# Optimization experiments

Measured on AMD Instinct MI355X. Metric: run time of the kernel, lower is better.

## Reference

```python
import jax, jax.numpy as jnp
import numpy as np

IGNORE = jnp.float32(-100000.0)

N_HEADS, D_MODEL, D_HEAD = 12, 768, 64


def setup_inputs() -> dict:
    key = jax.random.key(0)
    ks = jax.random.split(key, 5)
    B, S = 2, 2048
    std = 0.02
    x = jax.random.normal(ks[0], (B, S, D_MODEL), dtype=jnp.float32)
    W_Q = jax.random.normal(ks[1], (N_HEADS, D_MODEL, D_HEAD), dtype=jnp.float32) * std
    W_K = jax.random.normal(ks[2], (N_HEADS, D_MODEL, D_HEAD), dtype=jnp.float32) * std
    W_V = jax.random.normal(ks[3], (N_HEADS, D_MODEL, D_HEAD), dtype=jnp.float32) * std
    W_O = jax.random.normal(ks[4], (N_HEADS, D_HEAD, D_MODEL), dtype=jnp.float32) * std
    b_Q = jnp.zeros((N_HEADS, D_HEAD), dtype=jnp.float32)
    b_K = jnp.zeros((N_HEADS, D_HEAD), dtype=jnp.float32)
    b_V = jnp.zeros((N_HEADS, D_HEAD), dtype=jnp.float32)
    b_O = jnp.zeros((D_MODEL,), dtype=jnp.float32)
    return {"normalized_resid_pre": x, "W_Q": W_Q, "W_K": W_K, "W_V": W_V,
            "b_Q": b_Q, "b_K": b_K, "b_V": b_V, "W_O": W_O, "b_O": b_O}


def reference(normalized_resid_pre, W_Q, W_K, W_V, b_Q, b_K, b_V, W_O, b_O):
    x = normalized_resid_pre  # [b, s, d_model]
    q = jnp.einsum('bsd,hdk->bshk', x, W_Q) + b_Q  # [b, s, h, d_head]
    k = jnp.einsum('bsd,hdk->bshk', x, W_K) + b_K
    v = jnp.einsum('bsd,hdk->bshk', x, W_V) + b_V
    scores = jnp.einsum('bqhk,bkhd->bhqk'.replace('d', 'x').replace('x', 'k'),
                        q, k) if False else jnp.einsum('bihd,bjhd->bhij', q, k)
    scores = scores / jnp.sqrt(jnp.float32(q.shape[-1]))
    S = scores.shape[-1]
    causal = jnp.tril(jnp.ones((S, S), dtype=bool))  # True = keep
    scores = jnp.where(causal, scores, IGNORE)
    attn = jax.nn.softmax(scores, axis=-1)  # [b, h, q, k]
    z = jnp.einsum('bhij,bjhd->bihd', attn, v)  # [b, s, h, d_head]
    out = jnp.einsum('bihd,hdm->bim', z, W_O) + b_O  # [b, s, d_model]
    return out
```

## Files before the change

kernel.cpp:

```cpp
#include <hip/hip_runtime.h>


#define DEVINL __device__ __forceinline__

using bf16x8 = __attribute__((ext_vector_type(8))) __bf16;
using f32x4  = __attribute__((ext_vector_type(4))) float;

DEVINL unsigned short f32_bf16(float f) {
    unsigned u = __builtin_bit_cast(unsigned, f);
    return (unsigned short)((u + 0x7FFFu + ((u >> 16) & 1u)) >> 16);
}

DEVINL void gload16(const void* g, void* l) {
    __builtin_amdgcn_global_load_lds(
        (const __attribute__((address_space(1))) void*)g,
        (__attribute__((address_space(3))) void*)l, 16, 0, 0);
}

__global__ __launch_bounds__(256) void k_prep(const float* __restrict__ x,
                                              const float* __restrict__ Wq,
                                              const float* __restrict__ Wk,
                                              const float* __restrict__ Wv,
                                              const float* __restrict__ Wo,
                                              unsigned short* __restrict__ xb,
                                              unsigned short* __restrict__ wqkvT,
                                              unsigned short* __restrict__ woT) {
    __shared__ unsigned short tl[64][68];
    const int bid = blockIdx.x;
    const int t = threadIdx.x;
    if (bid < 3072) {
        int i = (bid * 256 + t) * 4;
        float4 v = *(const float4*)(x + i);
        ushort4 o;
        o.x = f32_bf16(v.x); o.y = f32_bf16(v.y); o.z = f32_bf16(v.z); o.w = f32_bf16(v.w);
        *(ushort4*)(xb + i) = o;
        return;
    }
    const int c = t & 63, r0 = t >> 6;
    if (bid < 3504) {
        const int sub = bid - 3072;
        const int tr = sub % 12, batch = sub / 12;
        const float* src = (batch < 12) ? Wq : (batch < 24) ? Wk : Wv;
        src += (size_t)(batch % 12) * 768 * 64;
        unsigned short* out = wqkvT + (size_t)batch * 64 * 768;
#pragma unroll
        for (int k = 0; k < 16; ++k) {
            int r = k * 4 + r0;
            tl[r][c] = f32_bf16(src[(size_t)(tr * 64 + r) * 64 + c]);
        }
        __syncthreads();
#pragma unroll
        for (int k = 0; k < 16; ++k) {
            int r2 = k * 4 + r0;
            out[(size_t)r2 * 768 + tr * 64 + c] = tl[c][r2];
        }
    } else {
        const int sub = bid - 3504;
        const int tr = sub % 12, tc = sub / 12;
#pragma unroll
        for (int k = 0; k < 16; ++k) {
            int r = k * 4 + r0;
            tl[r][c] = f32_bf16(Wo[(size_t)(tr * 64 + r) * 768 + tc * 64 + c]);
        }
        __syncthreads();
#pragma unroll
        for (int k = 0; k < 16; ++k) {
            int r2 = k * 4 + r0;
            woT[(size_t)(tc * 64 + r2) * 768 + tr * 64 + c] = tl[c][r2];
        }
    }
}

template <int BM, int BN, bool QKV>
__global__ __launch_bounds__(256) void k_gemm(const unsigned short* __restrict__ A,
                                              const unsigned short* __restrict__ BT,
                                              const float* __restrict__ b0,
                                              const float* __restrict__ b1,
                                              const float* __restrict__ b2,
                                              unsigned short* __restrict__ outb,
                                              unsigned short* __restrict__ vtb,
                                              float* __restrict__ outf) {
    constexpr int LDC = QKV ? 2304 : 768;
    constexpr int WM = BM / 2, WN = BN / 2, MR = WM / 16, NR = WN / 16;
    __shared__ alignas(16) unsigned short As[2][BM * 64];
    __shared__ alignas(16) unsigned short Bs[2][BN * 64];
    const int t = threadIdx.x;
    const int w = t >> 6, l = t & 63, lr = l & 15, lg = l >> 4;
    const int wr = (w >> 1) * WM, wc = (w & 1) * WN;
    const int m0 = blockIdx.y * BM;
    const int n0 = blockIdx.x * BN;

    auto stage = [&](int buf, int kt) {
        const int k0 = kt * 64;
#pragma unroll
        for (int i = 0; i < BM / 32; ++i) {
            const int s = i * 256 + t;
            const int row = s >> 3, cs = (s & 7) ^ (row & 7);
            gload16((const char*)A + ((size_t)(m0 + row) * 768 + k0) * 2 + cs * 16,
                    (char*)As[buf] + s * 16);
        }
#pragma unroll
        for (int i = 0; i < BN / 32; ++i) {
            const int s = i * 256 + t;
            const int row = s >> 3, cs = (s & 7) ^ (row & 7);
            gload16((const char*)BT + ((size_t)(n0 + row) * 768 + k0) * 2 + cs * 16,
                    (char*)Bs[buf] + s * 16);
        }
    };

    stage(0, 0);
    __syncthreads();

    f32x4 acc[MR][NR] = {};

    for (int kt = 0; kt < 12; ++kt) {
        const int cur = kt & 1;
        if (kt < 11) stage(cur ^ 1, kt + 1);

        bf16x8 af[MR][2], bfr[NR][2];
#pragma unroll
        for (int ri = 0; ri < MR; ++ri)
#pragma unroll
            for (int kk = 0; kk < 2; ++kk)
                af[ri][kk] = *(const bf16x8*)&As[cur][(wr + ri * 16 + lr) * 64 +
                                                     (((kk * 4 + lg) ^ (lr & 7)) << 3)];
#pragma unroll
        for (int cj = 0; cj < NR; ++cj)
#pragma unroll
            for (int kk = 0; kk < 2; ++kk)
                bfr[cj][kk] = *(const bf16x8*)&Bs[cur][(wc + cj * 16 + lr) * 64 +
                                                       (((kk * 4 + lg) ^ (lr & 7)) << 3)];
        __builtin_amdgcn_s_setprio(1);
#pragma unroll
        for (int ri = 0; ri < MR; ++ri)
#pragma unroll
            for (int cj = 0; cj < NR; ++cj) {
                acc[ri][cj] = __builtin_amdgcn_mfma_f32_16x16x32_bf16(
                    af[ri][0], bfr[cj][0], acc[ri][cj], 0, 0, 0);
                acc[ri][cj] = __builtin_amdgcn_mfma_f32_16x16x32_bf16(
                    af[ri][1], bfr[cj][1], acc[ri][cj], 0, 0, 0);
            }
        __builtin_amdgcn_s_setprio(0);
        __syncthreads();
    }

#pragma unroll
    for (int cj = 0; cj < NR; ++cj) {
        const int col = n0 + wc + cj * 16 + lr;
        if (QKV && col >= 1536) {
            const int vc = col - 1536;
            const float bv = b2[vc];
            const int hh = vc >> 6, dd = vc & 63;
#pragma unroll
            for (int ri = 0; ri < MR; ++ri) {
                const int row = m0 + wr + ri * 16 + lg * 4;
                const int bb = row >> 11, s = row & 2047;
                ushort4 pkv;
                pkv.x = f32_bf16(acc[ri][cj][0] + bv);
                pkv.y = f32_bf16(acc[ri][cj][1] + bv);
                pkv.z = f32_bf16(acc[ri][cj][2] + bv);
                pkv.w = f32_bf16(acc[ri][cj][3] + bv);
                *(ushort4*)(vtb + ((size_t)(bb * 12 + hh) * 64 + dd) * 2048 + s) = pkv;
            }
        } else {
            const float* bp = b0;
            int cc = col;
            if (QKV && col >= 768) { bp = b1; cc = col - 768; }
            const float bv = bp[cc];
            const float scl = (QKV && col < 768) ? 0.18033688011112042f : 1.0f;
#pragma unroll
            for (int ri = 0; ri < MR; ++ri)
#pragma unroll
                for (int e = 0; e < 4; ++e) {
                    const int row = m0 + wr + ri * 16 + lg * 4 + e;
                    const float v = (acc[ri][cj][e] + bv) * scl;
                    if (QKV) outb[(size_t)row * LDC + col] = f32_bf16(v);
                    else     outf[(size_t)row * LDC + col] = v;
                }
        }
    }
}

#define WREG 8704
__global__ __launch_bounds__(256) void k_flash(const unsigned short* __restrict__ qkv,
                                               const unsigned short* __restrict__ vtb,
                                               unsigned short* __restrict__ zb) {
    __shared__ alignas(16) char smem[4 * WREG + 1024];
    const int hb = blockIdx.x;
    const int h = hb % 12, b = hb / 12;
    const int p = blockIdx.y;
    const int qiA = 32 + p, qiB = 31 - p;
    const int q0A = qiA * 32, q0B = qiB * 32;
    const int nkvA = (qiA >> 1) + 1, nkvB = (qiB >> 1) + 1;
    const int t = threadIdx.x, w = t >> 6, l = t & 63, lr = l & 15, lg = l >> 4;

    char* p_w = smem + w * WREG;
    float* lldsA = (float*)(smem + 4 * WREG);
    float* lldsB = (float*)(smem + 4 * WREG + 512);

    const size_t qrowbase = (size_t)(b * 2048) * 2304;
    bf16x8 qfA[2][2], qfB[2][2];
#pragma unroll
    for (int ri = 0; ri < 2; ++ri)
#pragma unroll
        for (int kk = 0; kk < 2; ++kk) {
            qfA[ri][kk] = *(const bf16x8*)(qkv + qrowbase +
                                           (size_t)(q0A + ri * 16 + lr) * 2304 +
                                           h * 64 + kk * 32 + lg * 8);
            qfB[ri][kk] = *(const bf16x8*)(qkv + qrowbase +
                                           (size_t)(q0B + ri * 16 + lr) * 2304 +
                                           h * 64 + kk * 32 + lg * 8);
        }

    f32x4 oA[2][4] = {}, oB[2][4] = {};
    float lsA[2] = {0.f, 0.f}, lsB[2] = {0.f, 0.f};

    const unsigned short* kb = qkv + qrowbase + 768 + h * 64;
    const unsigned short* vt = vtb + (size_t)(b * 12 + h) * 64 * 2048;

    {
        bf16x8 kf[4][2];
        auto loadK = [&](int kv0) {
#pragma unroll
            for (int cj = 0; cj < 4; ++cj)
#pragma unroll
                for (int kk = 0; kk < 2; ++kk)
                    kf[cj][kk] = *(const bf16x8*)(kb + (size_t)(kv0 + cj * 16 + lr) * 2304 +
                                                  kk * 32 + lg * 8);
        };

        int kt = w;
        loadK(kt * 64);
        do {
            const int kv0 = kt * 64;

            bf16x8 vf[2][4];
#pragma unroll
            for (int kk = 0; kk < 2; ++kk)
#pragma unroll
                for (int dj = 0; dj < 4; ++dj)
                    vf[kk][dj] = *(const bf16x8*)(vt + (size_t)(dj * 16 + lr) * 2048 +
                                                  kv0 + kk * 32 + lg * 8);

            const f32x4 zz = {0.f, 0.f, 0.f, 0.f};

            if (kt < nkvB) {
                f32x4 st[2][4];
                __builtin_amdgcn_s_setprio(1);
#pragma unroll
                for (int ri = 0; ri < 2; ++ri)
#pragma unroll
                    for (int cj = 0; cj < 4; ++cj) {
                        f32x4 a0 = __builtin_amdgcn_mfma_f32_16x16x32_bf16(kf[cj][0], qfB[ri][0], zz, 0, 0, 0);
                        st[ri][cj] = __builtin_amdgcn_mfma_f32_16x16x32_bf16(kf[cj][1], qfB[ri][1], a0, 0, 0, 0);
                    }
                __builtin_amdgcn_s_setprio(0);

                if (kt == nkvB - 1) {
#pragma unroll
                    for (int ri = 0; ri < 2; ++ri)
#pragma unroll
                        for (int cj = 0; cj < 4; ++cj)
#pragma unroll
                            for (int e = 0; e < 4; ++e) {
                                const int kvv = kv0 + cj * 16 + lg * 4 + e;
                                const int qq  = q0B + ri * 16 + lr;
                                if (kvv > qq) st[ri][cj][e] = -1e30f;
                            }
                }

#pragma unroll
                for (int ri = 0; ri < 2; ++ri) {
                    float ps = 0.f;
#pragma unroll
                    for (int cj = 0; cj < 4; ++cj)
#pragma unroll
                        for (int e = 0; e < 4; ++e) {
                            const float pv = __builtin_amdgcn_exp2f(st[ri][cj][e]);
                            st[ri][cj][e] = pv;
                            ps += pv;
                        }
                    lsB[ri] += ps;

                    const int row = ri * 16 + lr;
#pragma unroll
                    for (int cj = 0; cj < 4; ++cj) {
                        unsigned lo, hi;
                        asm("v_cvt_pk_bf16_f32 %0, %1, %2"
                            : "=v"(lo) : "v"(st[ri][cj][0]), "v"(st[ri][cj][1]));
                        asm("v_cvt_pk_bf16_f32 %0, %1, %2"
                            : "=v"(hi) : "v"(st[ri][cj][2]), "v"(st[ri][cj][3]));
                        const int gr = (cj * 2 + (lg >> 1)) ^ (lr & 7);
                        uint2 pk2; pk2.x = lo; pk2.y = hi;
                        *(uint2*)(p_w + row * 128 + gr * 16 + (lg & 1) * 8) = pk2;
                    }
                }

                asm volatile("" ::: "memory");

                __builtin_amdgcn_s_setprio(1);
#pragma unroll
                for (int kk = 0; kk < 2; ++kk)
#pragma unroll
                    for (int ri = 0; ri < 2; ++ri) {
                        const int row = ri * 16 + lr;
                        const int g = (kk * 4 + lg) ^ (lr & 7);
                        bf16x8 pa = *(const bf16x8*)(p_w + row * 128 + g * 16);
#pragma unroll
                        for (int dj = 0; dj < 4; ++dj)
                            oB[ri][dj] = __builtin_amdgcn_mfma_f32_16x16x32_bf16(
                                vf[kk][dj], pa, oB[ri][dj], 0, 0, 0);
                    }
                __builtin_amdgcn_s_setprio(0);

                asm volatile("" ::: "memory");
            }

            {
                f32x4 st[2][4];
                __builtin_amdgcn_s_setprio(1);
#pragma unroll
                for (int ri = 0; ri < 2; ++ri)
#pragma unroll
                    for (int cj = 0; cj < 4; ++cj) {
                        f32x4 a0 = __builtin_amdgcn_mfma_f32_16x16x32_bf16(kf[cj][0], qfA[ri][0], zz, 0, 0, 0);
                        st[ri][cj] = __builtin_amdgcn_mfma_f32_16x16x32_bf16(kf[cj][1], qfA[ri][1], a0, 0, 0, 0);
                    }
                __builtin_amdgcn_s_setprio(0);

                if (kt == nkvA - 1) {
#pragma unroll
                    for (int ri = 0; ri < 2; ++ri)
#pragma unroll
                        for (int cj = 0; cj < 4; ++cj)
#pragma unroll
                            for (int e = 0; e < 4; ++e) {
                                const int kvv = kv0 + cj * 16 + lg * 4 + e;
                                const int qq  = q0A + ri * 16 + lr;
                                if (kvv > qq) st[ri][cj][e] = -1e30f;
                            }
                }

#pragma unroll
                for (int ri = 0; ri < 2; ++ri) {
                    float ps = 0.f;
#pragma unroll
                    for (int cj = 0; cj < 4; ++cj)
#pragma unroll
                        for (int e = 0; e < 4; ++e) {
                            const float pv = __builtin_amdgcn_exp2f(st[ri][cj][e]);
                            st[ri][cj][e] = pv;
                            ps += pv;
                        }
                    lsA[ri] += ps;

                    const int row = ri * 16 + lr;
#pragma unroll
                    for (int cj = 0; cj < 4; ++cj) {
                        unsigned lo, hi;
                        asm("v_cvt_pk_bf16_f32 %0, %1, %2"
                            : "=v"(lo) : "v"(st[ri][cj][0]), "v"(st[ri][cj][1]));
                        asm("v_cvt_pk_bf16_f32 %0, %1, %2"
                            : "=v"(hi) : "v"(st[ri][cj][2]), "v"(st[ri][cj][3]));
                        const int gr = (cj * 2 + (lg >> 1)) ^ (lr & 7);
                        uint2 pk2; pk2.x = lo; pk2.y = hi;
                        *(uint2*)(p_w + row * 128 + gr * 16 + (lg & 1) * 8) = pk2;
                    }
                }

                asm volatile("" ::: "memory");

                const bool more = (kt + 4 < nkvA);
                if (more) loadK(kv0 + 256);

                __builtin_amdgcn_s_setprio(1);
#pragma unroll
                for (int kk = 0; kk < 2; ++kk)
#pragma unroll
                    for (int ri = 0; ri < 2; ++ri) {
                        const int row = ri * 16 + lr;
                        const int g = (kk * 4 + lg) ^ (lr & 7);
                        bf16x8 pa = *(const bf16x8*)(p_w + row * 128 + g * 16);
#pragma unroll
                        for (int dj = 0; dj < 4; ++dj)
                            oA[ri][dj] = __builtin_amdgcn_mfma_f32_16x16x32_bf16(
                                vf[kk][dj], pa, oA[ri][dj], 0, 0, 0);
                    }
                __builtin_amdgcn_s_setprio(0);

                asm volatile("" ::: "memory");
            }

            kt += 4;
        } while (kt < nkvA);
    }

#pragma unroll
    for (int ri = 0; ri < 2; ++ri) {
        float a = lsA[ri];
        a += __shfl_xor(a, 16); a += __shfl_xor(a, 32);
        lsA[ri] = a;
        float bsum = lsB[ri];
        bsum += __shfl_xor(bsum, 16); bsum += __shfl_xor(bsum, 32);
        lsB[ri] = bsum;
    }
    if (lg == 0) {
#pragma unroll
        for (int ri = 0; ri < 2; ++ri) {
            lldsA[w * 32 + ri * 16 + lr] = lsA[ri];
            lldsB[w * 32 + ri * 16 + lr] = lsB[ri];
        }
    }
    __syncthreads();

#pragma unroll
    for (int item = 0; item < 2; ++item) {
        const float* lld = item ? lldsB : lldsA;
        const int q0 = item ? q0B : q0A;
        float* o_w = (float*)(smem + w * WREG);
#pragma unroll
        for (int ri = 0; ri < 2; ++ri) {
            const int row = ri * 16 + lr;
#pragma unroll
            for (int dj = 0; dj < 4; ++dj)
                *(f32x4*)&o_w[row * 68 + dj * 16 + lg * 4] = item ? oB[ri][dj] : oA[ri][dj];
        }
        __syncthreads();
        {
            const int row = w * 8 + (l >> 3);
            const int c0 = (l & 7) * 8;
            const float lt = lld[row] + lld[32 + row] + lld[64 + row] + lld[96 + row];
            const float inv = 1.0f / lt;
            ushort4 pk[2];
#pragma unroll
            for (int half = 0; half < 2; ++half) {
                unsigned short u[4];
#pragma unroll
                for (int k = 0; k < 4; ++k) {
                    float acc = 0.f;
#pragma unroll
                    for (int s = 0; s < 4; ++s)
                        acc += ((const float*)(smem + s * WREG))[row * 68 + c0 + half * 4 + k];
                    u[k] = f32_bf16(acc * inv);
                }
                pk[half] = make_ushort4(u[0], u[1], u[2], u[3]);
            }
            unsigned short* dst = zb + (size_t)(b * 2048 + q0 + row) * 768 + h * 64 + c0;
            *(ushort4*)dst = pk[0];
            *(ushort4*)(dst + 4) = pk[1];
        }
        __syncthreads();
    }
}

extern "C" void kernel_launch(void* const* d_in, const int* in_sizes, int n_in,
                              void* d_out, int out_size, void* d_ws, size_t ws_size,
                              hipStream_t stream) {
    (void)in_sizes; (void)n_in; (void)out_size; (void)ws_size;
    const float* x   = (const float*)d_in[0];
    const float* W_Q = (const float*)d_in[1];
    const float* W_K = (const float*)d_in[2];
    const float* W_V = (const float*)d_in[3];
    const float* b_Q = (const float*)d_in[4];
    const float* b_K = (const float*)d_in[5];
    const float* b_V = (const float*)d_in[6];
    const float* W_O = (const float*)d_in[7];
    const float* b_O = (const float*)d_in[8];
    float* out = (float*)d_out;

    char* ws = (char*)d_ws;
    unsigned short* xb    = (unsigned short*)(ws);
    unsigned short* qkvb  = (unsigned short*)(ws + 6291456);
    unsigned short* vtb   = (unsigned short*)(ws + 25165824);
    unsigned short* wqkvT = (unsigned short*)(ws + 31457280);
    unsigned short* woT   = (unsigned short*)(ws + 34996224);
    unsigned short* zb    = xb;

    k_prep<<<3648, 256, 0, stream>>>(x, W_Q, W_K, W_V, W_O, xb, wqkvT, woT);

    k_gemm<128, 64, true><<<dim3(36, 32), 256, 0, stream>>>(xb, wqkvT, b_Q, b_K, b_V,
                                                            qkvb, vtb, nullptr);

    k_flash<<<dim3(24, 32), 256, 0, stream>>>(qkvb, vtb, zb);

    k_gemm<64, 64, false><<<dim3(12, 64), 256, 0, stream>>>(zb, woT, b_O, b_O, b_O,
                                                            nullptr, nullptr, out);
}
```

Measured before the change: 95.59 us.

## Store K head-major and V in 8-row tiled layout for contiguous flash loads

```diff
diff --git a/kernel.cpp b/kernel.cpp
--- a/kernel.cpp
+++ b/kernel.cpp
@@ -77,10 +77,10 @@
                                               const float* __restrict__ b0,
                                               const float* __restrict__ b1,
                                               const float* __restrict__ b2,
-                                              unsigned short* __restrict__ outb,
+                                              unsigned short* __restrict__ qb,
+                                              unsigned short* __restrict__ khb,
                                               unsigned short* __restrict__ vtb,
                                               float* __restrict__ outf) {
-    constexpr int LDC = QKV ? 2304 : 768;
     constexpr int WM = BM / 2, WN = BN / 2, MR = WM / 16, NR = WN / 16;
     __shared__ alignas(16) unsigned short As[2][BM * 64];
     __shared__ alignas(16) unsigned short Bs[2][BN * 64];
@@ -160,29 +160,41 @@
                 pkv.y = f32_bf16(acc[ri][cj][1] + bv);
                 pkv.z = f32_bf16(acc[ri][cj][2] + bv);
                 pkv.w = f32_bf16(acc[ri][cj][3] + bv);
-                *(ushort4*)(vtb + ((size_t)(bb * 12 + hh) * 64 + dd) * 2048 + s) = pkv;
+                *(ushort4*)(vtb + (size_t)(bb * 12 + hh) * 131072 +
+                            (s >> 3) * 512 + dd * 8 + (s & 7)) = pkv;
             }
+        } else if (QKV && col >= 768) {
+            const int kc = col - 768;
+            const float bv = b1[kc];
+            const int hh = kc >> 6, dd = kc & 63;
+#pragma unroll
+            for (int ri = 0; ri < MR; ++ri)
+#pragma unroll
+                for (int e = 0; e < 4; ++e) {
+                    const int row = m0 + wr + ri * 16 + lg * 4 + e;
+                    const int bb = row >> 11, s = row & 2047;
+                    khb[(size_t)(bb * 12 + hh) * 131072 + s * 64 + dd] =
+                        f32_bf16(acc[ri][cj][e] + bv);
+                }
         } else {
-            const float* bp = b0;
-            int cc = col;
-            if (QKV && col >= 768) { bp = b1; cc = col - 768; }
-            const float bv = bp[cc];
-            const float scl = (QKV && col < 768) ? 0.18033688011112042f : 1.0f;
+            const float bv = b0[col];
+            const float scl = QKV ? 0.18033688011112042f : 1.0f;
 #pragma unroll
             for (int ri = 0; ri < MR; ++ri)
 #pragma unroll
                 for (int e = 0; e < 4; ++e) {
                     const int row = m0 + wr + ri * 16 + lg * 4 + e;
                     const float v = (acc[ri][cj][e] + bv) * scl;
-                    if (QKV) outb[(size_t)row * LDC + col] = f32_bf16(v);
-                    else     outf[(size_t)row * LDC + col] = v;
+                    if (QKV) qb[(size_t)row * 768 + col] = f32_bf16(v);
+                    else     outf[(size_t)row * 768 + col] = v;
                 }
         }
     }
 }
 
 #define WREG 8704
-__global__ __launch_bounds__(256) void k_flash(const unsigned short* __restrict__ qkv,
+__global__ __launch_bounds__(256) void k_flash(const unsigned short* __restrict__ qb,
+                                               const unsigned short* __restrict__ khb,
                                                const unsigned short* __restrict__ vtb,
                                                unsigned short* __restrict__ zb) {
     __shared__ alignas(16) char smem[4 * WREG + 1024];
@@ -198,25 +210,25 @@
     float* lldsA = (float*)(smem + 4 * WREG);
     float* lldsB = (float*)(smem + 4 * WREG + 512);
 
-    const size_t qrowbase = (size_t)(b * 2048) * 2304;
+    const size_t qrowbase = (size_t)(b * 2048) * 768;
     bf16x8 qfA[2][2], qfB[2][2];
 #pragma unroll
     for (int ri = 0; ri < 2; ++ri)
 #pragma unroll
         for (int kk = 0; kk < 2; ++kk) {
-            qfA[ri][kk] = *(const bf16x8*)(qkv + qrowbase +
-                                           (size_t)(q0A + ri * 16 + lr) * 2304 +
+            qfA[ri][kk] = *(const bf16x8*)(qb + qrowbase +
+                                           (size_t)(q0A + ri * 16 + lr) * 768 +
                                            h * 64 + kk * 32 + lg * 8);
-            qfB[ri][kk] = *(const bf16x8*)(qkv + qrowbase +
-                                           (size_t)(q0B + ri * 16 + lr) * 2304 +
+            qfB[ri][kk] = *(const bf16x8*)(qb + qrowbase +
+                                           (size_t)(q0B + ri * 16 + lr) * 768 +
                                            h * 64 + kk * 32 + lg * 8);
         }
 
     f32x4 oA[2][4] = {}, oB[2][4] = {};
     float lsA[2] = {0.f, 0.f}, lsB[2] = {0.f, 0.f};
 
-    const unsigned short* kb = qkv + qrowbase + 768 + h * 64;
-    const unsigned short* vt = vtb + (size_t)(b * 12 + h) * 64 * 2048;
+    const unsigned short* kh = khb + (size_t)(b * 12 + h) * 131072;
+    const unsigned short* vt = vtb + (size_t)(b * 12 + h) * 131072;
 
     {
         bf16x8 kf[4][2];
@@ -225,7 +237,7 @@
             for (int cj = 0; cj < 4; ++cj)
 #pragma unroll
                 for (int kk = 0; kk < 2; ++kk)
-                    kf[cj][kk] = *(const bf16x8*)(kb + (size_t)(kv0 + cj * 16 + lr) * 2304 +
+                    kf[cj][kk] = *(const bf16x8*)(kh + (size_t)(kv0 + cj * 16 + lr) * 64 +
                                                   kk * 32 + lg * 8);
         };
 
@@ -239,8 +251,8 @@
             for (int kk = 0; kk < 2; ++kk)
 #pragma unroll
                 for (int dj = 0; dj < 4; ++dj)
-                    vf[kk][dj] = *(const bf16x8*)(vt + (size_t)(dj * 16 + lr) * 2048 +
-                                                  kv0 + kk * 32 + lg * 8);
+                    vf[kk][dj] = *(const bf16x8*)(vt + (size_t)((kv0 >> 3) + kk * 4 + lg) * 512 +
+                                                  (dj * 16 + lr) * 8);
 
             const f32x4 zz = {0.f, 0.f, 0.f, 0.f};
 
@@ -470,7 +482,8 @@
 
     char* ws = (char*)d_ws;
     unsigned short* xb    = (unsigned short*)(ws);
-    unsigned short* qkvb  = (unsigned short*)(ws + 6291456);
+    unsigned short* qb    = (unsigned short*)(ws + 6291456);
+    unsigned short* khb   = (unsigned short*)(ws + 12582912);
     unsigned short* vtb   = (unsigned short*)(ws + 25165824);
     unsigned short* wqkvT = (unsigned short*)(ws + 31457280);
     unsigned short* woT   = (unsigned short*)(ws + 34996224);
@@ -479,10 +492,10 @@
     k_prep<<<3648, 256, 0, stream>>>(x, W_Q, W_K, W_V, W_O, xb, wqkvT, woT);
 
     k_gemm<128, 64, true><<<dim3(36, 32), 256, 0, stream>>>(xb, wqkvT, b_Q, b_K, b_V,
-                                                            qkvb, vtb, nullptr);
-
-    k_flash<<<dim3(24, 32), 256, 0, stream>>>(qkvb, vtb, zb);
+                                                            qb, khb, vtb, nullptr);
+
+    k_flash<<<dim3(24, 32), 256, 0, stream>>>(qb, khb, vtb, zb);
 
     k_gemm<64, 64, false><<<dim3(12, 64), 256, 0, stream>>>(zb, woT, b_O, b_O, b_O,
-                                                            nullptr, nullptr, out);
+                                                            nullptr, nullptr, nullptr, out);
 }
```

After: 85.77 us (median of 2 runs). 1.11x faster.
